# Kernel optimization log

Hardware: AMD Instinct MI355X
Metric: run time of the kernel (lower is better)

## Reference

```python
import jax, jax.numpy as jnp
import numpy as np

B, R, S, C, H, MLP = 4, 32, 4, 128, 4, 512  # batch, resolution, box_size, dim, heads, mlp_dim
N = S ** 3            # tokens per window = 64
NW = (R // S) ** 3    # windows per batch element = 512
SHIFT = S // 2


def _layernorm(x, g, b):
    m = jnp.mean(x, axis=-1, keepdims=True)
    v = jnp.var(x, axis=-1, keepdims=True)
    return (x - m) * jax.lax.rsqrt(v + 1e-5) * g + b


def _box_partition(x):
    # x: (b, R, R, R, C) -> (b*NW, N, C)
    b = x.shape[0]
    x = x.reshape(b, R // S, S, R // S, S, R // S, S, C)
    x = x.transpose(0, 1, 3, 5, 2, 4, 6, 7)
    return x.reshape(-1, N, C)


def _box_reverse(w, b):
    # w: (b*NW, N, C) -> (b, R, R, R, C)
    x = w.reshape(b, R // S, R // S, R // S, S, S, S, C)
    x = x.transpose(0, 1, 4, 2, 5, 3, 6, 7)
    return x.reshape(b, R, R, R, C)


def setup_inputs():
    key = jax.random.key(0)
    ks = jax.random.split(key, 8)
    f = lambda k, sh: jax.random.normal(k, sh, dtype=jnp.float32) * 0.02
    x = jax.random.normal(ks[0], (B, R ** 3, C), dtype=jnp.float32)
    qkv_w = f(ks[1], (3 * C, C))
    rpb_table = f(ks[2], ((3 * S - 1) ** 3, H))
    proj_w = f(ks[3], (C, C))
    proj_b = jnp.zeros((C,), jnp.float32)
    norm1_g = jnp.ones((C,), jnp.float32)
    norm1_b = jnp.zeros((C,), jnp.float32)
    norm2_g = jnp.ones((C,), jnp.float32)
    norm2_b = jnp.zeros((C,), jnp.float32)
    mlp_w1 = f(ks[4], (MLP, C))
    mlp_b1 = jnp.zeros((MLP,), jnp.float32)
    mlp_w2 = f(ks[5], (C, MLP))
    mlp_b2 = jnp.zeros((C,), jnp.float32)
    # relative position index (N, N), int constant
    coords = np.stack(np.meshgrid(*([np.arange(S)] * 3), indexing='ij')).reshape(3, -1)
    rel = coords[:, :, None] - coords[:, None, :]
    rel = rel.transpose(1, 2, 0) + (S - 1)
    rel[..., 0] *= (2 * S - 1) ** 2
    rel[..., 1] *= (2 * S - 1)
    rel_index = jnp.asarray(rel.sum(-1), jnp.int32)
    # shifted-window additive attention mask (NW, N, N)
    img = np.zeros((1, R, R, R, 1), np.float32)
    sl = (slice(0, -S), slice(-S, -SHIFT), slice(-SHIFT, None))
    cnt = 0
    for a in sl:
        for b2 in sl:
            for c in sl:
                img[:, a, b2, c, :] = cnt
                cnt += 1
    m = img.reshape(1, R // S, S, R // S, S, R // S, S, 1)
    m = m.transpose(0, 1, 3, 5, 2, 4, 6, 7).reshape(-1, N)
    am = m[:, None, :] - m[:, :, None]
    attn_mask = jnp.asarray(np.where(am != 0, -100.0, 0.0).astype(np.float32))
    return dict(x=x, qkv_w=qkv_w, rpb_table=rpb_table, proj_w=proj_w, proj_b=proj_b,
                norm1_g=norm1_g, norm1_b=norm1_b, norm2_g=norm2_g, norm2_b=norm2_b,
                mlp_w1=mlp_w1, mlp_b1=mlp_b1, mlp_w2=mlp_w2, mlp_b2=mlp_b2,
                attn_mask=attn_mask, rel_index=rel_index)


def reference(x, qkv_w, rpb_table, proj_w, proj_b, norm1_g, norm1_b,
              norm2_g, norm2_b, mlp_w1, mlp_b1, mlp_w2, mlp_b2,
              attn_mask, rel_index):
    scale = (C // H) ** -0.5
    shortcut = x
    xn = _layernorm(x, norm1_g, norm1_b).reshape(B, R, R, R, C)
    xs = jnp.roll(xn, (-SHIFT,) * 3, axis=(1, 2, 3))
    w = _box_partition(xs)  # (B*NW, N, C)
    qkv = (w @ qkv_w.T).reshape(-1, N, 3, H, C // H).transpose(2, 0, 3, 1, 4)
    q, k, v = qkv[0] * scale, qkv[1], qkv[2]  # (B*NW, H, N, hd)
    attn = jnp.einsum('whnd,whmd->whnm', q, k)
    bias = rpb_table[rel_index].transpose(2, 0, 1)  # (H, N, N)
    attn = attn + bias[None]
    attn = attn.reshape(B, NW, H, N, N) + attn_mask[None, :, None]
    attn = jax.nn.softmax(attn.reshape(-1, H, N, N), axis=-1)
    out = jnp.einsum('whnm,whmd->whnd', attn, v).transpose(0, 2, 1, 3).reshape(-1, N, C)
    out = out @ proj_w.T + proj_b
    xm = _box_reverse(out, B)
    xm = jnp.roll(xm, (SHIFT,) * 3, axis=(1, 2, 3)).reshape(B, -1, C)
    x1 = shortcut + 0.5 * xm
    h = _layernorm(x1, norm2_g, norm2_b)
    h = jax.nn.gelu(h @ mlp_w1.T + mlp_b1, approximate=False) @ mlp_w2.T + mlp_b2
    return x1 + 0.5 * h
```

## Files before the change

### kernel.cpp

```cpp
#include <hip/hip_runtime.h>
#include <hip/hip_bf16.h>

typedef unsigned short u16;
typedef unsigned int u32;
typedef short bf16x8 __attribute__((ext_vector_type(8)));
typedef float f32x4 __attribute__((ext_vector_type(4)));

__device__ __forceinline__ u16 f2bf(float f) {
  union { float f; u32 i; } v; v.f = f;
  u32 x = v.i;
  x += 0x7fff + ((x >> 16) & 1);
  return (u16)(x >> 16);
}
__device__ __forceinline__ u32 pack2(float a, float b) {
  return (u32)f2bf(a) | ((u32)f2bf(b) << 16);
}
__device__ __forceinline__ u32 cvtpk2(float a, float b) {
  __hip_bfloat162 t = __float22bfloat162_rn(float2{a, b});
  union { __hip_bfloat162 h; u32 u; } v; v.h = t; return v.u;
}


__global__ void prep_kernel(const float* __restrict__ rpb, const int* __restrict__ rel,
                            const float* __restrict__ qkv_w, const float* __restrict__ proj_w,
                            const float* __restrict__ w1, const float* __restrict__ w2,
                            float* __restrict__ bias, u16* __restrict__ qkv_f,
                            u16* __restrict__ proj_f, u16* __restrict__ w1f,
                            u16* __restrict__ w2f) {
  const int bid = blockIdx.x;
  if (bid < 64) {
    const int idx = bid * 256 + threadIdx.x;
    const int h = idx >> 12, rm = idx & 4095;
    bias[idx] = rpb[rel[rm] * 4 + h];
    return;
  }
  const int i4 = (bid - 64) * 256 + threadIdx.x;
  const int e = i4 * 4;
  const float scale = 0.17677669529663687f;
  float4 v; u16* dst;
  if (e < 49152) {
    v = *(const float4*)(qkv_w + e);
    if (e < 16384) { v.x *= scale; v.y *= scale; v.z *= scale; v.w *= scale; }
    const int row = e >> 7, col = e & 127;
    const int tile = (row >> 4) * 4 + (col >> 5);
    const int lane = ((col >> 3) & 3) * 16 + (row & 15);
    dst = qkv_f + tile * 512 + lane * 8 + (col & 7);
  } else if (e < 65536) {
    const int le = e - 49152;
    v = *(const float4*)(proj_w + le);
    const int row = le >> 7, col = le & 127;
    const int tile = (row >> 4) * 4 + (col >> 5);
    const int lane = ((col >> 3) & 3) * 16 + (row & 15);
    dst = proj_f + tile * 512 + lane * 8 + (col & 7);
  } else if (e < 131072) {
    const int le = e - 65536;
    v = *(const float4*)(w1 + le);
    const int row = le >> 7, col = le & 127;
    const int tile = (row >> 4) * 4 + (col >> 5);
    const int lane = ((col >> 3) & 3) * 16 + (row & 15);
    dst = w1f + tile * 512 + lane * 8 + (col & 7);
  } else {
    const int le = e - 131072;
    v = *(const float4*)(w2 + le);
    const int row = le >> 9, col = le & 511;
    const int tile = (row >> 4) * 16 + (col >> 5);
    const int lane = ((col >> 3) & 3) * 16 + (row & 15);
    dst = w2f + tile * 512 + lane * 8 + (col & 7);
  }
  *(uint2*)dst = make_uint2(pack2(v.x, v.y), pack2(v.z, v.w));
}

__global__ __launch_bounds__(512, 4) void attn_kernel(
    const float* __restrict__ x, const u16* __restrict__ qkv_f,
    const u16* __restrict__ proj_f, const float* __restrict__ proj_b,
    const float* __restrict__ n1g, const float* __restrict__ n1b,
    const float* __restrict__ amask, const float* __restrict__ bias,
    float* __restrict__ out)
{
  __shared__ __align__(16) unsigned char lds[70656];
  __shared__ int srcIdx[64];
  u16* xw = (u16*)(lds);
  u16* qb = (u16*)(lds + 17408);
  u16* kb = (u16*)(lds + 34816);
  u16* vt = (u16*)(lds + 52224);
  unsigned char* Pb = lds;
  u16* Ob = kb;

  const int tid = threadIdx.x;
  const int wv = tid >> 6, lane = tid & 63;
  const int l15 = lane & 15, lg = lane >> 4;
  const int hw = wv & 3;
  const int half = wv >> 2;

  const int wIdx = blockIdx.x;
  const int bb = wIdx >> 9, ww = wIdx & 511;
  const int w0 = ww >> 6, w1i = (ww >> 3) & 7, w2i = ww & 7;

  {
    const int tok = tid >> 3;
    const int qt = tid & 7;
    const int s0 = tok >> 4, s1 = (tok >> 2) & 3, s2 = tok & 3;
    const int p0 = (w0 * 4 + s0 + 2) & 31;
    const int p1 = (w1i * 4 + s1 + 2) & 31;
    const int p2 = (w2i * 4 + s2 + 2) & 31;
    const int src = (bb << 15) + (p0 << 10) + (p1 << 5) + p2;
    if (qt == 0) srcIdx[tok] = src;
    float v[16]; float s = 0.f, sq = 0.f;
    const float4* p4 = (const float4*)(x + src * 128 + qt * 16);
    #pragma unroll
    for (int i = 0; i < 4; ++i) {
      float4 u = p4[i];
      v[i * 4 + 0] = u.x; v[i * 4 + 1] = u.y; v[i * 4 + 2] = u.z; v[i * 4 + 3] = u.w;
      s += u.x + u.y + u.z + u.w;
      sq += u.x * u.x + u.y * u.y + u.z * u.z + u.w * u.w;
    }
    s  += __shfl_xor(s, 1);  s  += __shfl_xor(s, 2);  s  += __shfl_xor(s, 4);
    sq += __shfl_xor(sq, 1); sq += __shfl_xor(sq, 2); sq += __shfl_xor(sq, 4);
    const float mean = s * 0.0078125f;
    const float var  = sq * 0.0078125f - mean * mean;
    const float rstd = rsqrtf(var + 1e-5f);
    u16* dst = xw + tok * 136 + qt * 16;
    #pragma unroll
    for (int i = 0; i < 16; i += 2) {
      const int c = qt * 16 + i;
      float y0 = (v[i]     - mean) * rstd * n1g[c]     + n1b[c];
      float y1 = (v[i + 1] - mean) * rstd * n1g[c + 1] + n1b[c + 1];
      *(u32*)(dst + i) = cvtpk2(y0, y1);
    }
  }
  __syncthreads();

  const f32x4 zero4 = {0.f, 0.f, 0.f, 0.f};

  bf16x8 xa[2][4];
  #pragma unroll
  for (int ti = 0; ti < 2; ++ti)
    #pragma unroll
    for (int ks = 0; ks < 4; ++ks)
      xa[ti][ks] = *(const bf16x8*)(xw + ((half * 2 + ti) * 16 + l15) * 136 + ks * 32 + lg * 8);

  #pragma unroll
  for (int cc = 0; cc < 4; ++cc) {
    const u16* wp = qkv_f + (cc * 4 + hw) * 4 * 512 + lane * 8;
    f32x4 acc[2] = {zero4, zero4};
    #pragma unroll
    for (int ks = 0; ks < 4; ++ks) {
      const bf16x8 bfr = *(const bf16x8*)(wp + ks * 512);
      acc[0] = __builtin_amdgcn_mfma_f32_16x16x32_bf16(bfr, xa[0][ks], acc[0], 0, 0, 0);
      acc[1] = __builtin_amdgcn_mfma_f32_16x16x32_bf16(bfr, xa[1][ks], acc[1], 0, 0, 0);
    }
    u16* dstbuf = (cc < 2) ? qb : kb;
    const int ob = (cc & 1) * 64 + hw * 16 + lg * 4;
    #pragma unroll
    for (int ti = 0; ti < 2; ++ti) {
      const int token = (half * 2 + ti) * 16 + l15;
      uint2 pk = make_uint2(cvtpk2(acc[ti][0], acc[ti][1]), cvtpk2(acc[ti][2], acc[ti][3]));
      *(uint2*)(dstbuf + token * 136 + ob) = pk;
    }
  }
  #pragma unroll
  for (int cc = 4; cc < 6; ++cc) {
    const u16* wp = qkv_f + (cc * 4 + hw) * 4 * 512 + lane * 8;
    f32x4 acc[2] = {zero4, zero4};
    #pragma unroll
    for (int ks = 0; ks < 4; ++ks) {
      const bf16x8 bfr = *(const bf16x8*)(wp + ks * 512);
      acc[0] = __builtin_amdgcn_mfma_f32_16x16x32_bf16(xa[0][ks], bfr, acc[0], 0, 0, 0);
      acc[1] = __builtin_amdgcn_mfma_f32_16x16x32_bf16(xa[1][ks], bfr, acc[1], 0, 0, 0);
    }
    const int cvch = (cc - 4) * 64 + hw * 16 + l15;
    #pragma unroll
    for (int ti = 0; ti < 2; ++ti) {
      uint2 pk = make_uint2(cvtpk2(acc[ti][0], acc[ti][1]), cvtpk2(acc[ti][2], acc[ti][3]));
      *(uint2*)(vt + cvch * 72 + (half * 2 + ti) * 16 + lg * 4) = pk;
    }
  }
  __syncthreads();

  f32x4 s[2][4];
  {
    bf16x8 qa[2];
    #pragma unroll
    for (int ti = 0; ti < 2; ++ti)
      qa[ti] = *(const bf16x8*)(qb + ((half * 2 + ti) * 16 + l15) * 136 + hw * 32 + lg * 8);
    #pragma unroll
    for (int tj = 0; tj < 4; ++tj) {
      const bf16x8 kf = *(const bf16x8*)(kb + (tj * 16 + l15) * 136 + hw * 32 + lg * 8);
      s[0][tj] = __builtin_amdgcn_mfma_f32_16x16x32_bf16(qa[0], kf, zero4, 0, 0, 0);
      s[1][tj] = __builtin_amdgcn_mfma_f32_16x16x32_bf16(qa[1], kf, zero4, 0, 0, 0);
    }
  }
  #pragma unroll
  for (int ti = 0; ti < 2; ++ti) {
    #pragma unroll
    for (int r = 0; r < 4; ++r) {
      const int row = (half * 2 + ti) * 16 + lg * 4 + r;
      const float* bp = bias + hw * 4096 + row * 64;
      const float* mp = amask + ww * 4096 + row * 64;
      #pragma unroll
      for (int tj = 0; tj < 4; ++tj) {
        const int col = tj * 16 + l15;
        s[ti][tj][r] += bp[col] + mp[col];
      }
    }
  }
  __syncthreads();

  unsigned char* ps = Pb + wv * 4096;
  #pragma unroll
  for (int ti = 0; ti < 2; ++ti) {
    #pragma unroll
    for (int r = 0; r < 4; ++r) {
      float mx = fmaxf(fmaxf(s[ti][0][r], s[ti][1][r]), fmaxf(s[ti][2][r], s[ti][3][r]));
      mx = fmaxf(mx, __shfl_xor(mx, 1));
      mx = fmaxf(mx, __shfl_xor(mx, 2));
      mx = fmaxf(mx, __shfl_xor(mx, 4));
      mx = fmaxf(mx, __shfl_xor(mx, 8));
      float sum = 0.f;
      #pragma unroll
      for (int tj = 0; tj < 4; ++tj) {
        float e = __expf(s[ti][tj][r] - mx);
        s[ti][tj][r] = e; sum += e;
      }
      sum += __shfl_xor(sum, 1);
      sum += __shfl_xor(sum, 2);
      sum += __shfl_xor(sum, 4);
      sum += __shfl_xor(sum, 8);
      const float rcp = 1.0f / sum;
      const int row = ti * 16 + lg * 4 + r;
      const int swz = (row & 7) << 4;
      #pragma unroll
      for (int tj = 0; tj < 4; ++tj) {
        const int byteoff = (row * 128 + (tj * 16 + l15) * 2) ^ swz;
        *(u16*)(ps + byteoff) = f2bf(s[ti][tj][r] * rcp);
      }
    }
  }

  {
    f32x4 oacc[2][2] = {{zero4, zero4}, {zero4, zero4}};
    #pragma unroll
    for (int ks = 0; ks < 2; ++ks) {
      bf16x8 pa[2], vb[2];
      #pragma unroll
      for (int ti = 0; ti < 2; ++ti) {
        const int row = ti * 16 + l15;
        const int slot = ((ks * 4 + lg) ^ (row & 7)) << 4;
        pa[ti] = *(const bf16x8*)(ps + row * 128 + slot);
      }
      #pragma unroll
      for (int tj = 0; tj < 2; ++tj)
        vb[tj] = *(const bf16x8*)(vt + (hw * 32 + tj * 16 + l15) * 72 + ks * 32 + lg * 8);
      #pragma unroll
      for (int ti = 0; ti < 2; ++ti)
        #pragma unroll
        for (int tj = 0; tj < 2; ++tj)
          oacc[ti][tj] = __builtin_amdgcn_mfma_f32_16x16x32_bf16(vb[tj], pa[ti], oacc[ti][tj], 0, 0, 0);
    }
    #pragma unroll
    for (int ti = 0; ti < 2; ++ti)
      #pragma unroll
      for (int tj = 0; tj < 2; ++tj) {
        const int token = (half * 2 + ti) * 16 + l15;
        uint2 pk = make_uint2(cvtpk2(oacc[ti][tj][0], oacc[ti][tj][1]),
                              cvtpk2(oacc[ti][tj][2], oacc[ti][tj][3]));
        *(uint2*)(Ob + token * 136 + hw * 32 + tj * 16 + lg * 4) = pk;
      }
  }
  __syncthreads();

  bf16x8 oafr[2][4];
  #pragma unroll
  for (int ti = 0; ti < 2; ++ti)
    #pragma unroll
    for (int ks = 0; ks < 4; ++ks)
      oafr[ti][ks] = *(const bf16x8*)(Ob + ((half * 2 + ti) * 16 + l15) * 136 + ks * 32 + lg * 8);
  #pragma unroll
  for (int cc = 0; cc < 2; ++cc) {
    const u16* wp = proj_f + (cc * 4 + hw) * 4 * 512 + lane * 8;
    f32x4 acc[2] = {zero4, zero4};
    #pragma unroll
    for (int ks = 0; ks < 4; ++ks) {
      const bf16x8 bfr = *(const bf16x8*)(wp + ks * 512);
      acc[0] = __builtin_amdgcn_mfma_f32_16x16x32_bf16(bfr, oafr[0][ks], acc[0], 0, 0, 0);
      acc[1] = __builtin_amdgcn_mfma_f32_16x16x32_bf16(bfr, oafr[1][ks], acc[1], 0, 0, 0);
    }
    const int cb = cc * 64 + hw * 16 + lg * 4;
    const float4 pb4 = *(const float4*)(proj_b + cb);
    #pragma unroll
    for (int ti = 0; ti < 2; ++ti) {
      const int token = (half * 2 + ti) * 16 + l15;
      const int src = srcIdx[token];
      float4 xr = *(const float4*)(x + src * 128 + cb);
      xr.x += 0.5f * (acc[ti][0] + pb4.x);
      xr.y += 0.5f * (acc[ti][1] + pb4.y);
      xr.z += 0.5f * (acc[ti][2] + pb4.z);
      xr.w += 0.5f * (acc[ti][3] + pb4.w);
      *(float4*)(out + src * 128 + cb) = xr;
    }
  }
}

__global__ __launch_bounds__(256, 3) void mlp_kernel(
    const u16* __restrict__ w1f, const float* __restrict__ b1,
    const u16* __restrict__ w2f, const float* __restrict__ b2,
    const float* __restrict__ n2g, const float* __restrict__ n2b,
    float* __restrict__ out)
{
  __shared__ __align__(16) unsigned char lds[35840];
  u16* xn  = (u16*)(lds);
  u16* h1c0 = (u16*)(lds + 17408);
  u16* h1c1 = (u16*)(lds + 26624);

  const int tid = threadIdx.x;
  const int wave = tid >> 6, lane = tid & 63;
  const int l15 = lane & 15, lg = lane >> 4;
  const int base = blockIdx.x * 64;
  const f32x4 zero4 = {0.f, 0.f, 0.f, 0.f};

  {
    const int tl = tid >> 2;
    const int qt = tid & 3;
    const int tokg = base + tl;
    float v[32]; float s = 0.f, sq = 0.f;
    const float4* p4 = (const float4*)(out + tokg * 128 + qt * 32);
    #pragma unroll
    for (int i = 0; i < 8; ++i) {
      float4 u = p4[i];
      v[i * 4 + 0] = u.x; v[i * 4 + 1] = u.y; v[i * 4 + 2] = u.z; v[i * 4 + 3] = u.w;
      s += u.x + u.y + u.z + u.w;
      sq += u.x * u.x + u.y * u.y + u.z * u.z + u.w * u.w;
    }
    s  += __shfl_xor(s, 1);  s  += __shfl_xor(s, 2);
    sq += __shfl_xor(sq, 1); sq += __shfl_xor(sq, 2);
    const float mean = s * 0.0078125f;
    const float var  = sq * 0.0078125f - mean * mean;
    const float rstd = rsqrtf(var + 1e-5f);
    u16* dst = xn + tl * 136 + qt * 32;
    #pragma unroll
    for (int i = 0; i < 32; i += 2) {
      const int c = qt * 32 + i;
      float y0 = (v[i]     - mean) * rstd * n2g[c]     + n2b[c];
      float y1 = (v[i + 1] - mean) * rstd * n2g[c + 1] + n2b[c + 1];
      *(u32*)(dst + i) = cvtpk2(y0, y1);
    }
  }
  __syncthreads();

  bf16x8 xa[4][4];
  #pragma unroll
  for (int ti = 0; ti < 4; ++ti)
    #pragma unroll
    for (int ks = 0; ks < 4; ++ks)
      xa[ti][ks] = *(const bf16x8*)(xn + (ti * 16 + l15) * 136 + ks * 32 + lg * 8);

  f32x4 acc2[4][2];
  #pragma unroll
  for (int ti = 0; ti < 4; ++ti) { acc2[ti][0] = zero4; acc2[ti][1] = zero4; }

  #pragma unroll 1
  for (int oc = 0; oc < 8; ++oc) {
    u16* h1c = (oc & 1) ? h1c1 : h1c0;
    f32x4 a1[4];
    #pragma unroll
    for (int t = 0; t < 4; ++t) a1[t] = zero4;
    const u16* wp1 = w1f + (oc * 4 + wave) * 4 * 512 + lane * 8;
    #pragma unroll
    for (int ks = 0; ks < 4; ++ks) {
      const bf16x8 bfr = *(const bf16x8*)(wp1 + ks * 512);
      #pragma unroll
      for (int ti = 0; ti < 4; ++ti)
        a1[ti] = __builtin_amdgcn_mfma_f32_16x16x32_bf16(bfr, xa[ti][ks], a1[ti], 0, 0, 0);
    }
    bf16x8 w2r[2][2];
    #pragma unroll
    for (int tj = 0; tj < 2; ++tj)
      #pragma unroll
      for (int ks = 0; ks < 2; ++ks)
        w2r[tj][ks] = *(const bf16x8*)(w2f + (((wave * 2 + tj) * 16) + (oc * 2 + ks)) * 512 + lane * 8);

    const int olb = wave * 16 + lg * 4;
    const float4 b14 = *(const float4*)(b1 + oc * 64 + olb);
    const float b1v[4] = {b14.x, b14.y, b14.z, b14.w};
    #pragma unroll
    for (int ti = 0; ti < 4; ++ti) {
      float g[4];
      #pragma unroll
      for (int r = 0; r < 4; ++r) {
        const float u = a1[ti][r] + b1v[r];
        const float t = u + 0.044715f * u * u * u;
        g[r] = u / (1.0f + __expf(-1.5957691216057308f * t));
      }
      const int token = ti * 16 + l15;
      *(uint2*)(h1c + token * 72 + olb) = make_uint2(cvtpk2(g[0], g[1]), cvtpk2(g[2], g[3]));
    }
    __syncthreads();

    #pragma unroll
    for (int ks = 0; ks < 2; ++ks) {
      bf16x8 afr[4];
      #pragma unroll
      for (int ti = 0; ti < 4; ++ti)
        afr[ti] = *(const bf16x8*)(h1c + (ti * 16 + l15) * 72 + ks * 32 + lg * 8);
      #pragma unroll
      for (int ti = 0; ti < 4; ++ti)
        #pragma unroll
        for (int tj = 0; tj < 2; ++tj)
          acc2[ti][tj] = __builtin_amdgcn_mfma_f32_16x16x32_bf16(w2r[tj][ks], afr[ti], acc2[ti][tj], 0, 0, 0);
    }
  }

  #pragma unroll
  for (int tj = 0; tj < 2; ++tj) {
    const int cb = wave * 32 + tj * 16 + lg * 4;
    const float4 b24 = *(const float4*)(b2 + cb);
    #pragma unroll
    for (int ti = 0; ti < 4; ++ti) {
      const int tokg = base + ti * 16 + l15;
      float4 o4 = *(float4*)(out + tokg * 128 + cb);
      o4.x += 0.5f * (acc2[ti][tj][0] + b24.x);
      o4.y += 0.5f * (acc2[ti][tj][1] + b24.y);
      o4.z += 0.5f * (acc2[ti][tj][2] + b24.z);
      o4.w += 0.5f * (acc2[ti][tj][3] + b24.w);
      *(float4*)(out + tokg * 128 + cb) = o4;
    }
  }
}

extern "C" void kernel_launch(void* const* d_in, const int* in_sizes, int n_in,
                              void* d_out, int out_size, void* d_ws, size_t ws_size,
                              hipStream_t stream) {
  const float* x      = (const float*)d_in[0];
  const float* qkv_w  = (const float*)d_in[1];
  const float* rpb    = (const float*)d_in[2];
  const float* proj_w = (const float*)d_in[3];
  const float* proj_b = (const float*)d_in[4];
  const float* n1g    = (const float*)d_in[5];
  const float* n1b    = (const float*)d_in[6];
  const float* n2g    = (const float*)d_in[7];
  const float* n2b    = (const float*)d_in[8];
  const float* w1     = (const float*)d_in[9];
  const float* b1     = (const float*)d_in[10];
  const float* w2     = (const float*)d_in[11];
  const float* b2     = (const float*)d_in[12];
  const float* amask  = (const float*)d_in[13];
  const int*   rel    = (const int*)d_in[14];
  float* out  = (float*)d_out;

  unsigned char* ws = (unsigned char*)d_ws;
  float* bias = (float*)(ws);
  u16* qkv_f  = (u16*)(ws + 65536);
  u16* proj_f = (u16*)(ws + 163840);
  u16* w1f    = (u16*)(ws + 196608);
  u16* w2f    = (u16*)(ws + 327680);

  prep_kernel<<<256, 256, 0, stream>>>(rpb, rel, qkv_w, proj_w, w1, w2,
                                       bias, qkv_f, proj_f, w1f, w2f);
  attn_kernel<<<2048, 512, 0, stream>>>(x, qkv_f, proj_f, proj_b, n1g, n1b, amask, bias, out);
  mlp_kernel<<<2048, 256, 0, stream>>>(w1f, b1, w2f, b2, n2g, n2b, out);
}
```

Baseline: 164.6 us.

## Restructure MLP kernel so each wave owns 16 tokens, using shuffles instead of LDS

The MLP kernel is repartitioned so each wave handles its own 16 tokens across all output channels, rather than a slice of channels across all 64 tokens. The GELU hidden activations are rearranged between lanes with shuffles to form MFMA B operands, which removes the hidden-activation LDS buffers and the per-chunk __syncthreads. Shared memory shrinks enough to raise launch bounds to 4 blocks per SM. In exchange, each wave now loads every W1/W2 weight fragment itself (four times more global/L2 weight traffic per block) and pays for extra shuffle instructions.

```diff
diff --git a/kernel.cpp b/kernel.cpp
--- a/kernel.cpp
+++ b/kernel.cpp
@@ -301,19 +301,17 @@
   }
 }
 
-__global__ __launch_bounds__(256, 3) void mlp_kernel(
+__global__ __launch_bounds__(256, 4) void mlp_kernel(
     const u16* __restrict__ w1f, const float* __restrict__ b1,
     const u16* __restrict__ w2f, const float* __restrict__ b2,
     const float* __restrict__ n2g, const float* __restrict__ n2b,
     float* __restrict__ out)
 {
-  __shared__ __align__(16) unsigned char lds[35840];
-  u16* xn  = (u16*)(lds);
-  u16* h1c0 = (u16*)(lds + 17408);
-  u16* h1c1 = (u16*)(lds + 26624);
+  __shared__ __align__(16) unsigned char lds[17408];
+  u16* xn = (u16*)(lds);
 
   const int tid = threadIdx.x;
-  const int wave = tid >> 6, lane = tid & 63;
+  const int wv = tid >> 6, lane = tid & 63;
   const int l15 = lane & 15, lg = lane >> 4;
   const int base = blockIdx.x * 64;
   const f32x4 zero4 = {0.f, 0.f, 0.f, 0.f};
@@ -345,85 +343,94 @@
       *(u32*)(dst + i) = cvtpk2(y0, y1);
     }
   }
-  __syncthreads();
-
-  bf16x8 xa[4][4];
-  #pragma unroll
-  for (int ti = 0; ti < 4; ++ti)
-    #pragma unroll
-    for (int ks = 0; ks < 4; ++ks)
-      xa[ti][ks] = *(const bf16x8*)(xn + (ti * 16 + l15) * 136 + ks * 32 + lg * 8);
-
-  f32x4 acc2[4][2];
-  #pragma unroll
-  for (int ti = 0; ti < 4; ++ti) { acc2[ti][0] = zero4; acc2[ti][1] = zero4; }
+
+  bf16x8 xa[4];
+  #pragma unroll
+  for (int ks = 0; ks < 4; ++ks)
+    xa[ks] = *(const bf16x8*)(xn + (wv * 16 + l15) * 136 + ks * 32 + lg * 8);
+
+  f32x4 acc2[8];
+  #pragma unroll
+  for (int ct = 0; ct < 8; ++ct) acc2[ct] = zero4;
+
+  const int src01 = l15 + ((lg & 1) << 5);
+  const int src23 = src01 + 16;
+  const int hiSel = lg >> 1;
 
   #pragma unroll 1
   for (int oc = 0; oc < 8; ++oc) {
-    u16* h1c = (oc & 1) ? h1c1 : h1c0;
     f32x4 a1[4];
     #pragma unroll
-    for (int t = 0; t < 4; ++t) a1[t] = zero4;
-    const u16* wp1 = w1f + (oc * 4 + wave) * 4 * 512 + lane * 8;
-    #pragma unroll
-    for (int ks = 0; ks < 4; ++ks) {
-      const bf16x8 bfr = *(const bf16x8*)(wp1 + ks * 512);
-      #pragma unroll
-      for (int ti = 0; ti < 4; ++ti)
-        a1[ti] = __builtin_amdgcn_mfma_f32_16x16x32_bf16(bfr, xa[ti][ks], a1[ti], 0, 0, 0);
-    }
-    bf16x8 w2r[2][2];
-    #pragma unroll
-    for (int tj = 0; tj < 2; ++tj)
-      #pragma unroll
-      for (int ks = 0; ks < 2; ++ks)
-        w2r[tj][ks] = *(const bf16x8*)(w2f + (((wave * 2 + tj) * 16) + (oc * 2 + ks)) * 512 + lane * 8);
-
-    const int olb = wave * 16 + lg * 4;
-    const float4 b14 = *(const float4*)(b1 + oc * 64 + olb);
-    const float b1v[4] = {b14.x, b14.y, b14.z, b14.w};
-    #pragma unroll
-    for (int ti = 0; ti < 4; ++ti) {
+    for (int ot = 0; ot < 4; ++ot) a1[ot] = zero4;
+    #pragma unroll
+    for (int ot = 0; ot < 4; ++ot) {
+      const u16* wp1 = w1f + ((oc * 4 + ot) * 4) * 512 + lane * 8;
+      #pragma unroll
+      for (int ks = 0; ks < 4; ++ks) {
+        const bf16x8 bfr = *(const bf16x8*)(wp1 + ks * 512);
+        a1[ot] = __builtin_amdgcn_mfma_f32_16x16x32_bf16(bfr, xa[ks], a1[ot], 0, 0, 0);
+      }
+    }
+    bf16x8 w2a[8];
+    #pragma unroll
+    for (int ct = 0; ct < 8; ++ct)
+      w2a[ct] = *(const bf16x8*)(w2f + (ct * 16 + 2 * oc) * 512 + lane * 8);
+
+    u32 pk[4][2];
+    #pragma unroll
+    for (int ot = 0; ot < 4; ++ot) {
+      const float4 b14 = *(const float4*)(b1 + oc * 64 + ot * 16 + lg * 4);
+      const float bv[4] = {b14.x, b14.y, b14.z, b14.w};
       float g[4];
       #pragma unroll
-      for (int r = 0; r < 4; ++r) {
-        const float u = a1[ti][r] + b1v[r];
+      for (int q = 0; q < 4; ++q) {
+        const float u = a1[ot][q] + bv[q];
         const float t = u + 0.044715f * u * u * u;
-        g[r] = u / (1.0f + __expf(-1.5957691216057308f * t));
-      }
-      const int token = ti * 16 + l15;
-      *(uint2*)(h1c + token * 72 + olb) = make_uint2(cvtpk2(g[0], g[1]), cvtpk2(g[2], g[3]));
-    }
-    __syncthreads();
-
+        g[q] = u / (1.0f + __expf(-1.5957691216057308f * t));
+      }
+      pk[ot][0] = cvtpk2(g[0], g[1]);
+      pk[ot][1] = cvtpk2(g[2], g[3]);
+    }
+
+    u32 bw[2][4];
     #pragma unroll
     for (int ks = 0; ks < 2; ++ks) {
-      bf16x8 afr[4];
-      #pragma unroll
-      for (int ti = 0; ti < 4; ++ti)
-        afr[ti] = *(const bf16x8*)(h1c + (ti * 16 + l15) * 72 + ks * 32 + lg * 8);
-      #pragma unroll
-      for (int ti = 0; ti < 4; ++ti)
-        #pragma unroll
-        for (int tj = 0; tj < 2; ++tj)
-          acc2[ti][tj] = __builtin_amdgcn_mfma_f32_16x16x32_bf16(w2r[tj][ks], afr[ti], acc2[ti][tj], 0, 0, 0);
-    }
-  }
-
-  #pragma unroll
-  for (int tj = 0; tj < 2; ++tj) {
-    const int cb = wave * 32 + tj * 16 + lg * 4;
+      #pragma unroll
+      for (int j = 0; j < 4; ++j) {
+        const int srcLane = (j < 2) ? src01 : src23;
+        const int lo = __shfl((int)pk[2 * ks][j & 1], srcLane, 64);
+        const int hi = __shfl((int)pk[2 * ks + 1][j & 1], srcLane, 64);
+        bw[ks][j] = hiSel ? (u32)hi : (u32)lo;
+      }
+    }
+    bf16x8 bf0, bf1;
+    __builtin_memcpy(&bf0, &bw[0][0], 16);
+    __builtin_memcpy(&bf1, &bw[1][0], 16);
+
+    bf16x8 w2b[8];
+    #pragma unroll
+    for (int ct = 0; ct < 8; ++ct)
+      w2b[ct] = *(const bf16x8*)(w2f + (ct * 16 + 2 * oc + 1) * 512 + lane * 8);
+
+    #pragma unroll
+    for (int ct = 0; ct < 8; ++ct)
+      acc2[ct] = __builtin_amdgcn_mfma_f32_16x16x32_bf16(w2a[ct], bf0, acc2[ct], 0, 0, 0);
+    #pragma unroll
+    for (int ct = 0; ct < 8; ++ct)
+      acc2[ct] = __builtin_amdgcn_mfma_f32_16x16x32_bf16(w2b[ct], bf1, acc2[ct], 0, 0, 0);
+  }
+
+  const int tokg = base + wv * 16 + l15;
+  #pragma unroll
+  for (int ct = 0; ct < 8; ++ct) {
+    const int cb = ct * 16 + lg * 4;
     const float4 b24 = *(const float4*)(b2 + cb);
-    #pragma unroll
-    for (int ti = 0; ti < 4; ++ti) {
-      const int tokg = base + ti * 16 + l15;
-      float4 o4 = *(float4*)(out + tokg * 128 + cb);
-      o4.x += 0.5f * (acc2[ti][tj][0] + b24.x);
-      o4.y += 0.5f * (acc2[ti][tj][1] + b24.y);
-      o4.z += 0.5f * (acc2[ti][tj][2] + b24.z);
-      o4.w += 0.5f * (acc2[ti][tj][3] + b24.w);
-      *(float4*)(out + tokg * 128 + cb) = o4;
-    }
+    float4 o4 = *(float4*)(out + tokg * 128 + cb);
+    o4.x += 0.5f * (acc2[ct][0] + b24.x);
+    o4.y += 0.5f * (acc2[ct][1] + b24.y);
+    o4.z += 0.5f * (acc2[ct][2] + b24.z);
+    o4.w += 0.5f * (acc2[ct][3] + b24.w);
+    *(float4*)(out + tokg * 128 + cb) = o4;
   }
 }
 
```

Result: slower. 201.2 us (+22.2%).
